# Kernel tuning notes

Hardware: AMD Instinct MI355X
Metric: run time of the kernel (lower is better)

The kernel has to match this reference:

```python
import jax, jax.numpy as jnp
import numpy as np

B, T, E, H = 2, 2048, 1024, 16
Dh = E // H  # head_size = 64


def setup_inputs() -> dict:
    key = jax.random.key(0)
    ks = jax.random.split(key, 6)
    s = E ** -0.5
    x = jax.random.normal(ks[0], (B, T, E), dtype=jnp.float32)
    Wq = jax.random.normal(ks[1], (H, E, Dh), dtype=jnp.float32) * s
    Wk = jax.random.normal(ks[2], (H, E, Dh), dtype=jnp.float32) * s
    Wv = jax.random.normal(ks[3], (H, E, Dh), dtype=jnp.float32) * s
    wo_w = jax.random.normal(ks[4], (E, E), dtype=jnp.float32) * s  # torch Linear weight [out,in]
    wo_b = jax.random.normal(ks[5], (E,), dtype=jnp.float32) * 0.01
    return {"x": x, "Wq": Wq, "Wk": Wk, "Wv": Wv, "wo_w": wo_w, "wo_b": wo_b}


def reference(x, Wq, Wk, Wv, wo_w, wo_b):
    # Batched equivalent of the per-head Python loop: project all heads at once.
    q = jnp.einsum('bte,hed->bhtd', x, Wq)
    k = jnp.einsum('bte,hed->bhtd', x, Wk)
    v = jnp.einsum('bte,hed->bhtd', x, Wv)
    scale = Dh ** -0.5
    scores = jnp.einsum('bhtd,bhsd->bhts', q, k) * scale  # [B,H,T,T]
    causal = jnp.tril(jnp.ones((T, T), dtype=bool))
    scores = jnp.where(causal, scores, jnp.finfo(scores.dtype).min)
    att = jax.nn.softmax(scores, axis=-1)
    out = jnp.einsum('bhts,bhsd->bhtd', att, v)  # [B,H,T,Dh]
    # concat heads (head order along last dim, matching torch.cat over heads)
    out = out.transpose(0, 2, 1, 3).reshape(B, T, E)
    return out @ wo_w.T + wo_b
```

## Files before the change

kernel.cpp:

```cpp
#include <hip/hip_runtime.h>

#define B_ 2
#define T_ 2048
#define E_ 1024
#define H_ 16
#define DH 64

typedef unsigned short u16;
typedef unsigned int u32;
typedef __bf16 bf16x8 __attribute__((ext_vector_type(8)));
typedef float f32x4 __attribute__((ext_vector_type(4)));

__device__ __forceinline__ u16 f2bf(float f) {
  u32 u = __builtin_bit_cast(u32, f);
  u = u + 0x7FFFu + ((u >> 16) & 1u);
  return (u16)(u >> 16);
}
__device__ __forceinline__ float bf2f(u16 v) {
  return __builtin_bit_cast(float, (u32)v << 16);
}
__device__ __forceinline__ bf16x8 ldfrag(const u16* p) { return *(const bf16x8*)p; }

__device__ __forceinline__ void gload_lds16(const u16* g, u16* l) {
  __builtin_amdgcn_global_load_lds((const __attribute__((address_space(1))) u32*)g,
                                   (__attribute__((address_space(3))) u32*)l, 16, 0, 0);
}

__global__ void k_conv_x(const float* __restrict__ src, u16* __restrict__ dst) {
  u32 i = (blockIdx.x * 256u + threadIdx.x) * 8u;
  float4 a = *(const float4*)(src + i);
  float4 b = *(const float4*)(src + i + 4);
  uint4 v;
  v.x = (u32)f2bf(a.x) | ((u32)f2bf(a.y) << 16);
  v.y = (u32)f2bf(a.z) | ((u32)f2bf(a.w) << 16);
  v.z = (u32)f2bf(b.x) | ((u32)f2bf(b.y) << 16);
  v.w = (u32)f2bf(b.z) | ((u32)f2bf(b.w) << 16);
  *(uint4*)(dst + i) = v;
}

__global__ __launch_bounds__(256) void k_conv_wT(const float* __restrict__ Wq, const float* __restrict__ Wk,
                                                 const float* __restrict__ Wv, u16* __restrict__ wT) {
  __shared__ __align__(16) u16 Ls[64][68];
  const int t = threadIdx.x;
  const int e0 = blockIdx.x * 64;
  const int h = blockIdx.y;
  const int which = blockIdx.z;
  const float* src = (which == 0) ? Wq : ((which == 1) ? Wk : Wv);
  const float scale = (which == 0) ? 0.18033688011112042f : 1.0f;
#pragma unroll
  for (int p = 0; p < 4; p++) {
    int idx = p * 256 + t;
    int row = idx >> 4, ch = idx & 15;
    float4 v = *(const float4*)(src + ((size_t)h * E_ + e0 + row) * DH + ch * 4);
    uint2 pk;
    pk.x = (u32)f2bf(v.x * scale) | ((u32)f2bf(v.y * scale) << 16);
    pk.y = (u32)f2bf(v.z * scale) | ((u32)f2bf(v.w * scale) << 16);
    *(uint2*)(&Ls[row][ch * 4]) = pk;
  }
  __syncthreads();
  u16* dst = wT + ((size_t)which * H_ + h) * (DH * E_);
#pragma unroll
  for (int p = 0; p < 4; p++) {
    int idx = p * 256 + t;
    int d = idx >> 4, ec = idx & 15;
    uint2 pk;
    pk.x = (u32)Ls[ec * 4 + 0][d] | ((u32)Ls[ec * 4 + 1][d] << 16);
    pk.y = (u32)Ls[ec * 4 + 2][d] | ((u32)Ls[ec * 4 + 3][d] << 16);
    *(uint2*)(dst + (size_t)d * E_ + e0 + ec * 4) = pk;
  }
}

__global__ __launch_bounds__(256, 3) void k_qkv(const u16* __restrict__ xb, const u16* __restrict__ wT,
                                                u16* __restrict__ Qb, u16* __restrict__ Kb,
                                                u16* __restrict__ VbT) {
  __shared__ __align__(16) u16 As[128 * 64];
  __shared__ __align__(16) u16 Bs[128 * 64];
  const int tid = threadIdx.x;
  const int w = tid >> 6, lane = tid & 63, quad = lane >> 4, lr = lane & 15;
  const int wr = w >> 1, wc = w & 1;
  const int t0 = blockIdx.x * 128;
  const int n0 = blockIdx.y * 128;
  const int sr = lane >> 3, sc = lane & 7;

  f32x4 acc[4][4];
  const f32x4 z4 = {0.f, 0.f, 0.f, 0.f};
#pragma unroll
  for (int i = 0; i < 4; i++)
#pragma unroll
    for (int j = 0; j < 4; j++) acc[i][j] = z4;

  for (int k0 = 0; k0 < E_; k0 += 64) {
    __syncthreads();
#pragma unroll
    for (int ii = 0; ii < 4; ii++) {
      int ra = w * 32 + ii * 8 + sr;
      gload_lds16(xb + (size_t)(t0 + ra) * E_ + k0 + ((sc ^ (ra & 7)) << 3),
                  As + (w * 32 + ii * 8) * 64);
      gload_lds16(wT + (size_t)(n0 + ra) * E_ + k0 + ((sc ^ (ra & 7)) << 3),
                  Bs + (w * 32 + ii * 8) * 64);
    }
    __syncthreads();
#pragma unroll
    for (int kk = 0; kk < 2; kk++) {
      bf16x8 af[4], bfv[4];
#pragma unroll
      for (int rt = 0; rt < 4; rt++) {
        int row = wr * 64 + rt * 16 + lr;
        af[rt] = ldfrag(As + row * 64 + (((kk * 4 + quad) ^ (row & 7)) << 3));
      }
#pragma unroll
      for (int ct = 0; ct < 4; ct++) {
        int row = wc * 64 + ct * 16 + lr;
        bfv[ct] = ldfrag(Bs + row * 64 + (((kk * 4 + quad) ^ (row & 7)) << 3));
      }
#pragma unroll
      for (int rt = 0; rt < 4; rt++)
#pragma unroll
        for (int ct = 0; ct < 4; ct++)
          acc[rt][ct] = __builtin_amdgcn_mfma_f32_16x16x32_bf16(af[rt], bfv[ct], acc[rt][ct], 0, 0, 0);
    }
  }

  const int qkv = n0 >> 10;
  if (qkv < 2) {
    u16* outp = (qkv == 0) ? Qb : Kb;
#pragma unroll
    for (int rt = 0; rt < 4; rt++)
#pragma unroll
      for (int ct = 0; ct < 4; ct++) {
        int n = n0 + wc * 64 + ct * 16 + lr;
        int h = (n >> 6) & 15, d = n & 63;
#pragma unroll
        for (int r = 0; r < 4; r++) {
          int t = t0 + wr * 64 + rt * 16 + quad * 4 + r;
          int bb = t >> 11, tt = t & 2047;
          outp[(((size_t)bb * H_ + h) * T_ + tt) * DH + d] = f2bf(acc[rt][ct][r]);
        }
      }
  } else {
#pragma unroll
    for (int rt = 0; rt < 4; rt++)
#pragma unroll
      for (int ct = 0; ct < 4; ct++) {
        int n = n0 + wc * 64 + ct * 16 + lr;
        int h = (n >> 6) & 15, d = n & 63;
        int t = t0 + wr * 64 + rt * 16 + quad * 4;
        int bb = t >> 11, tt = t & 2047;
        uint2 pk;
        pk.x = (u32)f2bf(acc[rt][ct][0]) | ((u32)f2bf(acc[rt][ct][1]) << 16);
        pk.y = (u32)f2bf(acc[rt][ct][2]) | ((u32)f2bf(acc[rt][ct][3]) << 16);
        *(uint2*)(VbT + (((size_t)bb * H_ + h) * DH + d) * T_ + tt) = pk;
      }
  }
}

__global__ __launch_bounds__(256, 4) void k_attn(const u16* __restrict__ Qb, const u16* __restrict__ Kb,
                                                 const u16* __restrict__ VbT, u16* __restrict__ O0,
                                                 u16* __restrict__ O1, float* __restrict__ Mb,
                                                 float* __restrict__ Lb) {
  __shared__ __align__(16) u16 Qs[64 * 64];
  __shared__ __align__(16) u16 Ks[64 * 64];
  __shared__ __align__(16) u16 Vts[64 * 64];
  __shared__ __align__(16) u16 Ps[64 * 64];
  const int tid = threadIdx.x;
  const int w = tid >> 6, lane = tid & 63, quad = lane >> 4, lr = lane & 15;
  const int l7 = lr & 7;
  const int srow = lane >> 3, schunk = lane & 7;
  const int i = blockIdx.x >> 1, s = blockIdx.x & 1;
  const int h = blockIdx.y, bb = blockIdx.z;
  const u16* qb = Qb + ((size_t)bb * H_ + h) * (size_t)(T_ * DH);
  const u16* kb = Kb + ((size_t)bb * H_ + h) * (size_t)(T_ * DH);
  const u16* vbT = VbT + ((size_t)bb * H_ + h) * (size_t)(T_ * DH);
  const f32x4 z4 = {0.f, 0.f, 0.f, 0.f};

  for (int jb = 0; jb < 2; jb++) {
    const int qt = jb ? i : (31 - i);
    const int sg = jb ? (1 - s) : s;
    const int t0 = qt * 64;
    __syncthreads();
#pragma unroll
    for (int ii = 0; ii < 2; ii++) {
      int r = w * 16 + ii * 8 + srow;
      gload_lds16(qb + (size_t)(t0 + r) * DH + ((schunk ^ (r & 7)) << 3),
                  Qs + (w * 16 + ii * 8) * 64);
    }

    f32x4 o_acc[4];
#pragma unroll
    for (int dt = 0; dt < 4; dt++) o_acc[dt] = z4;
    float m_i = -__builtin_inff(), l_i = 0.f;

    for (int jt = sg; jt <= qt; jt += 2) {
      const int j0 = jt * 64;
      __syncthreads();
#pragma unroll
      for (int ii = 0; ii < 2; ii++) {
        int r = w * 16 + ii * 8 + srow;
        gload_lds16(kb + (size_t)(j0 + r) * DH + ((schunk ^ (r & 7)) << 3),
                    Ks + (w * 16 + ii * 8) * 64);
        gload_lds16(vbT + (size_t)r * T_ + j0 + ((schunk ^ (r & 7)) << 3),
                    Vts + (w * 16 + ii * 8) * 64);
      }
      __syncthreads();

      f32x4 s_acc[4];
#pragma unroll
      for (int st = 0; st < 4; st++) s_acc[st] = z4;
#pragma unroll
      for (int kk = 0; kk < 2; kk++) {
        bf16x8 bq = ldfrag(Qs + (w * 16 + lr) * 64 + (((kk * 4 + quad) ^ l7) << 3));
#pragma unroll
        for (int st = 0; st < 4; st++) {
          bf16x8 ak = ldfrag(Ks + (st * 16 + lr) * 64 + (((kk * 4 + quad) ^ l7) << 3));
          s_acc[st] = __builtin_amdgcn_mfma_f32_16x16x32_bf16(ak, bq, s_acc[st], 0, 0, 0);
        }
      }

      if (jt == qt) {
        int qloc = w * 16 + lr;
#pragma unroll
        for (int st = 0; st < 4; st++) {
          int sbase = st * 16 + quad * 4;
#pragma unroll
          for (int r = 0; r < 4; r++)
            if (sbase + r > qloc) s_acc[st][r] = -__builtin_inff();
        }
      }

      float v01 = fmaxf(fmaxf(s_acc[0][0], s_acc[0][1]), fmaxf(s_acc[0][2], s_acc[0][3]));
      float v23 = fmaxf(fmaxf(s_acc[1][0], s_acc[1][1]), fmaxf(s_acc[1][2], s_acc[1][3]));
      float v45 = fmaxf(fmaxf(s_acc[2][0], s_acc[2][1]), fmaxf(s_acc[2][2], s_acc[2][3]));
      float v67 = fmaxf(fmaxf(s_acc[3][0], s_acc[3][1]), fmaxf(s_acc[3][2], s_acc[3][3]));
      float v = fmaxf(fmaxf(v01, v23), fmaxf(v45, v67));
      v = fmaxf(v, __shfl_xor(v, 16));
      v = fmaxf(v, __shfl_xor(v, 32));
      float mnew = fmaxf(m_i, v);
      float alpha = __builtin_amdgcn_exp2f(m_i - mnew);
      m_i = mnew;
      float rsum = 0.f;
#pragma unroll
      for (int st = 0; st < 4; st++) {
        float p0 = __builtin_amdgcn_exp2f(s_acc[st][0] - m_i);
        float p1 = __builtin_amdgcn_exp2f(s_acc[st][1] - m_i);
        float p2 = __builtin_amdgcn_exp2f(s_acc[st][2] - m_i);
        float p3 = __builtin_amdgcn_exp2f(s_acc[st][3] - m_i);
        rsum += (p0 + p1) + (p2 + p3);
        uint2 pk;
        pk.x = (__builtin_bit_cast(u32, p0) >> 16) | (__builtin_bit_cast(u32, p1) & 0xffff0000u);
        pk.y = (__builtin_bit_cast(u32, p2) >> 16) | (__builtin_bit_cast(u32, p3) & 0xffff0000u);
        *(uint2*)(Ps + (w * 16 + lr) * 64 + (((st * 2 + (quad >> 1)) ^ l7) << 3) + ((quad & 1) << 2)) = pk;
      }
      rsum += __shfl_xor(rsum, 16);
      rsum += __shfl_xor(rsum, 32);
      l_i = l_i * alpha + rsum;
#pragma unroll
      for (int dt = 0; dt < 4; dt++)
#pragma unroll
        for (int r = 0; r < 4; r++) o_acc[dt][r] *= alpha;

#pragma unroll
      for (int kk = 0; kk < 2; kk++) {
        bf16x8 bp = ldfrag(Ps + (w * 16 + lr) * 64 + (((kk * 4 + quad) ^ l7) << 3));
#pragma unroll
        for (int dt = 0; dt < 4; dt++) {
          bf16x8 av = ldfrag(Vts + (dt * 16 + lr) * 64 + (((kk * 4 + quad) ^ l7) << 3));
          o_acc[dt] = __builtin_amdgcn_mfma_f32_16x16x32_bf16(av, bp, o_acc[dt], 0, 0, 0);
        }
      }
    }

    u16* op = (sg == 0) ? O0 : O1;
    float inv = (l_i > 0.f) ? (1.0f / l_i) : 0.f;
    int t = t0 + w * 16 + lr;
    u16* orow = op + ((size_t)bb * T_ + t) * E_ + h * DH;
#pragma unroll
    for (int dt = 0; dt < 4; dt++) {
      uint2 pk;
      pk.x = (u32)f2bf(o_acc[dt][0] * inv) | ((u32)f2bf(o_acc[dt][1] * inv) << 16);
      pk.y = (u32)f2bf(o_acc[dt][2] * inv) | ((u32)f2bf(o_acc[dt][3] * inv) << 16);
      *(uint2*)(orow + dt * 16 + quad * 4) = pk;
    }
    if (quad == 0) {
      int idx = ((sg * B_ + bb) * H_ + h) * T_ + t;
      Mb[idx] = m_i;
      Lb[idx] = l_i;
    }
  }
}

__global__ void k_combine(u16* __restrict__ AO, const u16* __restrict__ O1,
                          const float* __restrict__ Mb, const float* __restrict__ Lb) {
  int idx = blockIdx.x * 256 + threadIdx.x;
  int e0 = idx * 4;
  int bb = e0 >> 21, t = (e0 >> 10) & 2047, hh = (e0 >> 6) & 15;
  int r0 = (bb * H_ + hh) * T_ + t;
  int r1 = r0 + B_ * H_ * T_;
  float m0 = Mb[r0], l0 = Lb[r0], m1 = Mb[r1], l1 = Lb[r1];
  float m = fmaxf(m0, m1);
  float w0 = l0 * __builtin_amdgcn_exp2f(m0 - m);
  float w1 = l1 * __builtin_amdgcn_exp2f(m1 - m);
  float inv = 1.0f / (w0 + w1);
  float a0 = w0 * inv, a1 = w1 * inv;
  uint2 u0 = *(const uint2*)(AO + e0);
  uint2 u1 = *(const uint2*)(O1 + e0);
  float f0 = a0 * bf2f((u16)u0.x) + a1 * bf2f((u16)u1.x);
  float f1 = a0 * bf2f((u16)(u0.x >> 16)) + a1 * bf2f((u16)(u1.x >> 16));
  float f2 = a0 * bf2f((u16)u0.y) + a1 * bf2f((u16)u1.y);
  float f3 = a0 * bf2f((u16)(u0.y >> 16)) + a1 * bf2f((u16)(u1.y >> 16));
  uint2 o;
  o.x = (u32)f2bf(f0) | ((u32)f2bf(f1) << 16);
  o.y = (u32)f2bf(f2) | ((u32)f2bf(f3) << 16);
  *(uint2*)(AO + e0) = o;
}

__global__ __launch_bounds__(256, 3) void k_oproj(const u16* __restrict__ AO, const u16* __restrict__ woB,
                                                  const float* __restrict__ bias, float* __restrict__ out) {
  __shared__ __align__(16) u16 As[128 * 64];
  __shared__ __align__(16) u16 Bs[128 * 64];
  const int tid = threadIdx.x;
  const int w = tid >> 6, lane = tid & 63, quad = lane >> 4, lr = lane & 15;
  const int wr = w >> 1, wc = w & 1;
  const int r0 = blockIdx.x * 128, n0 = blockIdx.y * 128;
  const int sr = lane >> 3, sc = lane & 7;

  f32x4 acc[4][4];
  const f32x4 z4 = {0.f, 0.f, 0.f, 0.f};
#pragma unroll
  for (int i = 0; i < 4; i++)
#pragma unroll
    for (int j = 0; j < 4; j++) acc[i][j] = z4;

  for (int k0 = 0; k0 < E_; k0 += 64) {
    __syncthreads();
#pragma unroll
    for (int ii = 0; ii < 4; ii++) {
      int ra = w * 32 + ii * 8 + sr;
      gload_lds16(AO + (size_t)(r0 + ra) * E_ + k0 + ((sc ^ (ra & 7)) << 3),
                  As + (w * 32 + ii * 8) * 64);
      gload_lds16(woB + (size_t)(n0 + ra) * E_ + k0 + ((sc ^ (ra & 7)) << 3),
                  Bs + (w * 32 + ii * 8) * 64);
    }
    __syncthreads();
#pragma unroll
    for (int kk = 0; kk < 2; kk++) {
      bf16x8 af[4], bfv[4];
#pragma unroll
      for (int rt = 0; rt < 4; rt++) {
        int row = wr * 64 + rt * 16 + lr;
        af[rt] = ldfrag(As + row * 64 + (((kk * 4 + quad) ^ (row & 7)) << 3));
      }
#pragma unroll
      for (int ct = 0; ct < 4; ct++) {
        int row = wc * 64 + ct * 16 + lr;
        bfv[ct] = ldfrag(Bs + row * 64 + (((kk * 4 + quad) ^ (row & 7)) << 3));
      }
#pragma unroll
      for (int rt = 0; rt < 4; rt++)
#pragma unroll
        for (int ct = 0; ct < 4; ct++)
          acc[rt][ct] = __builtin_amdgcn_mfma_f32_16x16x32_bf16(af[rt], bfv[ct], acc[rt][ct], 0, 0, 0);
    }
  }

#pragma unroll
  for (int ct = 0; ct < 4; ct++) {
    float bv = bias[n0 + wc * 64 + ct * 16 + lr];
#pragma unroll
    for (int rt = 0; rt < 4; rt++)
#pragma unroll
      for (int r = 0; r < 4; r++) {
        int row = r0 + wr * 64 + rt * 16 + quad * 4 + r;
        out[(size_t)row * E_ + n0 + wc * 64 + ct * 16 + lr] = acc[rt][ct][r] + bv;
      }
  }
}

extern "C" void kernel_launch(void* const* d_in, const int* in_sizes, int n_in,
                              void* d_out, int out_size, void* d_ws, size_t ws_size,
                              hipStream_t stream) {
  const float* x = (const float*)d_in[0];
  const float* Wq = (const float*)d_in[1];
  const float* Wk = (const float*)d_in[2];
  const float* Wv = (const float*)d_in[3];
  const float* wo_w = (const float*)d_in[4];
  const float* wo_b = (const float*)d_in[5];
  float* out = (float*)d_out;
  char* ws = (char*)d_ws;

  u16* xb  = (u16*)(ws + 0);
  u16* wT  = (u16*)(ws + 8388608);
  u16* woB = (u16*)(ws + 14680064);
  u16* Qb  = (u16*)(ws + 16777216);
  u16* Kb  = (u16*)(ws + 25165824);
  u16* VbT = (u16*)(ws + 33554432);
  u16* AO  = (u16*)(ws + 41943040);
  u16* O1  = xb;
  float* Mb = (float*)(ws + 8388608);
  float* Lb = (float*)(ws + 8912896);

  k_conv_x<<<2048, 256, 0, stream>>>(x, xb);
  k_conv_wT<<<dim3(16, 16, 3), 256, 0, stream>>>(Wq, Wk, Wv, wT);
  k_conv_x<<<512, 256, 0, stream>>>(wo_w, woB);
  k_qkv<<<dim3(32, 24), 256, 0, stream>>>(xb, wT, Qb, Kb, VbT);
  k_attn<<<dim3(32, 16, 2), 256, 0, stream>>>(Qb, Kb, VbT, AO, O1, Mb, Lb);
  k_combine<<<4096, 256, 0, stream>>>(AO, O1, Mb, Lb);
  k_oproj<<<dim3(32, 8), 256, 0, stream>>>(AO, woB, wo_b, out);
}
```

Measured before the change: 181.2 us.

## Fuse conversion kernels, double-buffer K/V in attention, shrink oproj tiles

Merges the three fp32-to-bf16 conversion launches into one kernel that picks its role from the block index, removing two launches. The attention kernel now loads Q fragments straight from global memory into registers. K/V tiles are double-buffered in LDS so the next tile's load overlaps the current tile's compute. The output projection uses 64x128 tiles with 512 blocks instead of 256, giving better CU fill at the cost of less reuse per block. The larger LDS footprint in attention may reduce occupancy.

```diff
diff --git a/kernel.cpp b/kernel.cpp
--- a/kernel.cpp
+++ b/kernel.cpp
@@ -26,31 +26,40 @@
                                    (__attribute__((address_space(3))) u32*)l, 16, 0, 0);
 }
 
-__global__ void k_conv_x(const float* __restrict__ src, u16* __restrict__ dst) {
-  u32 i = (blockIdx.x * 256u + threadIdx.x) * 8u;
-  float4 a = *(const float4*)(src + i);
-  float4 b = *(const float4*)(src + i + 4);
-  uint4 v;
-  v.x = (u32)f2bf(a.x) | ((u32)f2bf(a.y) << 16);
-  v.y = (u32)f2bf(a.z) | ((u32)f2bf(a.w) << 16);
-  v.z = (u32)f2bf(b.x) | ((u32)f2bf(b.y) << 16);
-  v.w = (u32)f2bf(b.z) | ((u32)f2bf(b.w) << 16);
-  *(uint4*)(dst + i) = v;
-}
-
-__global__ __launch_bounds__(256) void k_conv_wT(const float* __restrict__ Wq, const float* __restrict__ Wk,
-                                                 const float* __restrict__ Wv, u16* __restrict__ wT) {
+__global__ __launch_bounds__(256) void k_conv_all(const float* __restrict__ x,
+                                                  const float* __restrict__ Wq,
+                                                  const float* __restrict__ Wk,
+                                                  const float* __restrict__ Wv,
+                                                  const float* __restrict__ wo_w,
+                                                  u16* __restrict__ xb, u16* __restrict__ wT,
+                                                  u16* __restrict__ woB) {
   __shared__ __align__(16) u16 Ls[64][68];
   const int t = threadIdx.x;
-  const int e0 = blockIdx.x * 64;
-  const int h = blockIdx.y;
-  const int which = blockIdx.z;
+  const int bx = blockIdx.x;
+  if (bx < 2048 || bx >= 2816) {
+    const float* src = (bx < 2048) ? x : wo_w;
+    u16* dst = (bx < 2048) ? xb : woB;
+    u32 i = (((bx < 2048) ? bx : (bx - 2816)) * 256u + t) * 8u;
+    float4 a = *(const float4*)(src + i);
+    float4 b = *(const float4*)(src + i + 4);
+    uint4 v;
+    v.x = (u32)f2bf(a.x) | ((u32)f2bf(a.y) << 16);
+    v.y = (u32)f2bf(a.z) | ((u32)f2bf(a.w) << 16);
+    v.z = (u32)f2bf(b.x) | ((u32)f2bf(b.y) << 16);
+    v.w = (u32)f2bf(b.z) | ((u32)f2bf(b.w) << 16);
+    *(uint4*)(dst + i) = v;
+    return;
+  }
+  const int idx = bx - 2048;
+  const int e0 = (idx & 15) * 64;
+  const int h = (idx >> 4) & 15;
+  const int which = idx >> 8;
   const float* src = (which == 0) ? Wq : ((which == 1) ? Wk : Wv);
   const float scale = (which == 0) ? 0.18033688011112042f : 1.0f;
 #pragma unroll
   for (int p = 0; p < 4; p++) {
-    int idx = p * 256 + t;
-    int row = idx >> 4, ch = idx & 15;
+    int id2 = p * 256 + t;
+    int row = id2 >> 4, ch = id2 & 15;
     float4 v = *(const float4*)(src + ((size_t)h * E_ + e0 + row) * DH + ch * 4);
     uint2 pk;
     pk.x = (u32)f2bf(v.x * scale) | ((u32)f2bf(v.y * scale) << 16);
@@ -61,8 +70,8 @@
   u16* dst = wT + ((size_t)which * H_ + h) * (DH * E_);
 #pragma unroll
   for (int p = 0; p < 4; p++) {
-    int idx = p * 256 + t;
-    int d = idx >> 4, ec = idx & 15;
+    int id2 = p * 256 + t;
+    int d = id2 >> 4, ec = id2 & 15;
     uint2 pk;
     pk.x = (u32)Ls[ec * 4 + 0][d] | ((u32)Ls[ec * 4 + 1][d] << 16);
     pk.y = (u32)Ls[ec * 4 + 2][d] | ((u32)Ls[ec * 4 + 3][d] << 16);
@@ -158,10 +167,8 @@
                                                  const u16* __restrict__ VbT, u16* __restrict__ O0,
                                                  u16* __restrict__ O1, float* __restrict__ Mb,
                                                  float* __restrict__ Lb) {
-  __shared__ __align__(16) u16 Qs[64 * 64];
-  __shared__ __align__(16) u16 Ks[64 * 64];
-  __shared__ __align__(16) u16 Vts[64 * 64];
-  __shared__ __align__(16) u16 Ps[64 * 64];
+  __shared__ __align__(16) u16 KV[2][8192];
+  __shared__ __align__(16) u16 Ps[4096];
   const int tid = threadIdx.x;
   const int w = tid >> 6, lane = tid & 63, quad = lane >> 4, lr = lane & 15;
   const int l7 = lr & 7;
@@ -178,42 +185,54 @@
     const int sg = jb ? (1 - s) : s;
     const int t0 = qt * 64;
     __syncthreads();
-#pragma unroll
-    for (int ii = 0; ii < 2; ii++) {
-      int r = w * 16 + ii * 8 + srow;
-      gload_lds16(qb + (size_t)(t0 + r) * DH + ((schunk ^ (r & 7)) << 3),
-                  Qs + (w * 16 + ii * 8) * 64);
-    }
+
+    const u16* qrow = qb + (size_t)(t0 + w * 16 + lr) * DH;
+    bf16x8 bq0 = ldfrag(qrow + quad * 8);
+    bf16x8 bq1 = ldfrag(qrow + 32 + quad * 8);
 
     f32x4 o_acc[4];
 #pragma unroll
     for (int dt = 0; dt < 4; dt++) o_acc[dt] = z4;
     float m_i = -__builtin_inff(), l_i = 0.f;
 
-    for (int jt = sg; jt <= qt; jt += 2) {
-      const int j0 = jt * 64;
-      __syncthreads();
+    int cur = 0;
+    if (sg <= qt) {
+      int j0 = sg * 64;
 #pragma unroll
       for (int ii = 0; ii < 2; ii++) {
         int r = w * 16 + ii * 8 + srow;
         gload_lds16(kb + (size_t)(j0 + r) * DH + ((schunk ^ (r & 7)) << 3),
-                    Ks + (w * 16 + ii * 8) * 64);
+                    KV[0] + (w * 16 + ii * 8) * 64);
         gload_lds16(vbT + (size_t)r * T_ + j0 + ((schunk ^ (r & 7)) << 3),
-                    Vts + (w * 16 + ii * 8) * 64);
-      }
+                    KV[0] + 4096 + (w * 16 + ii * 8) * 64);
+      }
+    }
+
+    for (int jt = sg; jt <= qt; jt += 2) {
       __syncthreads();
+      if (jt + 2 <= qt) {
+        int j0n = (jt + 2) * 64;
+#pragma unroll
+        for (int ii = 0; ii < 2; ii++) {
+          int r = w * 16 + ii * 8 + srow;
+          gload_lds16(kb + (size_t)(j0n + r) * DH + ((schunk ^ (r & 7)) << 3),
+                      KV[cur ^ 1] + (w * 16 + ii * 8) * 64);
+          gload_lds16(vbT + (size_t)r * T_ + j0n + ((schunk ^ (r & 7)) << 3),
+                      KV[cur ^ 1] + 4096 + (w * 16 + ii * 8) * 64);
+        }
+      }
+      const u16* Ks = KV[cur];
+      const u16* Vts = KV[cur] + 4096;
 
       f32x4 s_acc[4];
 #pragma unroll
       for (int st = 0; st < 4; st++) s_acc[st] = z4;
 #pragma unroll
-      for (int kk = 0; kk < 2; kk++) {
-        bf16x8 bq = ldfrag(Qs + (w * 16 + lr) * 64 + (((kk * 4 + quad) ^ l7) << 3));
-#pragma unroll
-        for (int st = 0; st < 4; st++) {
-          bf16x8 ak = ldfrag(Ks + (st * 16 + lr) * 64 + (((kk * 4 + quad) ^ l7) << 3));
-          s_acc[st] = __builtin_amdgcn_mfma_f32_16x16x32_bf16(ak, bq, s_acc[st], 0, 0, 0);
-        }
+      for (int st = 0; st < 4; st++) {
+        bf16x8 ak0 = ldfrag(Ks + (st * 16 + lr) * 64 + ((quad ^ l7) << 3));
+        bf16x8 ak1 = ldfrag(Ks + (st * 16 + lr) * 64 + (((4 + quad) ^ l7) << 3));
+        s_acc[st] = __builtin_amdgcn_mfma_f32_16x16x32_bf16(ak0, bq0, s_acc[st], 0, 0, 0);
+        s_acc[st] = __builtin_amdgcn_mfma_f32_16x16x32_bf16(ak1, bq1, s_acc[st], 0, 0, 0);
       }
 
       if (jt == qt) {
@@ -267,6 +286,7 @@
           o_acc[dt] = __builtin_amdgcn_mfma_f32_16x16x32_bf16(av, bp, o_acc[dt], 0, 0, 0);
         }
       }
+      cur ^= 1;
     }
 
     u16* op = (sg == 0) ? O0 : O1;
@@ -313,64 +333,68 @@
   *(uint2*)(AO + e0) = o;
 }
 
-__global__ __launch_bounds__(256, 3) void k_oproj(const u16* __restrict__ AO, const u16* __restrict__ woB,
+__global__ __launch_bounds__(256, 2) void k_oproj(const u16* __restrict__ AO, const u16* __restrict__ woB,
                                                   const float* __restrict__ bias, float* __restrict__ out) {
-  __shared__ __align__(16) u16 As[128 * 64];
+  __shared__ __align__(16) u16 As[64 * 64];
   __shared__ __align__(16) u16 Bs[128 * 64];
   const int tid = threadIdx.x;
   const int w = tid >> 6, lane = tid & 63, quad = lane >> 4, lr = lane & 15;
-  const int wr = w >> 1, wc = w & 1;
-  const int r0 = blockIdx.x * 128, n0 = blockIdx.y * 128;
+  const int r0 = blockIdx.x * 64, n0 = blockIdx.y * 128;
   const int sr = lane >> 3, sc = lane & 7;
 
-  f32x4 acc[4][4];
+  f32x4 acc[4][2];
   const f32x4 z4 = {0.f, 0.f, 0.f, 0.f};
 #pragma unroll
   for (int i = 0; i < 4; i++)
 #pragma unroll
-    for (int j = 0; j < 4; j++) acc[i][j] = z4;
+    for (int j = 0; j < 2; j++) acc[i][j] = z4;
 
   for (int k0 = 0; k0 < E_; k0 += 64) {
     __syncthreads();
 #pragma unroll
+    for (int ii = 0; ii < 2; ii++) {
+      int ra = w * 16 + ii * 8 + sr;
+      gload_lds16(AO + (size_t)(r0 + ra) * E_ + k0 + ((sc ^ (ra & 7)) << 3),
+                  As + (w * 16 + ii * 8) * 64);
+    }
+#pragma unroll
     for (int ii = 0; ii < 4; ii++) {
-      int ra = w * 32 + ii * 8 + sr;
-      gload_lds16(AO + (size_t)(r0 + ra) * E_ + k0 + ((sc ^ (ra & 7)) << 3),
-                  As + (w * 32 + ii * 8) * 64);
-      gload_lds16(woB + (size_t)(n0 + ra) * E_ + k0 + ((sc ^ (ra & 7)) << 3),
+      int rb = w * 32 + ii * 8 + sr;
+      gload_lds16(woB + (size_t)(n0 + rb) * E_ + k0 + ((sc ^ (rb & 7)) << 3),
                   Bs + (w * 32 + ii * 8) * 64);
     }
     __syncthreads();
 #pragma unroll
     for (int kk = 0; kk < 2; kk++) {
-      bf16x8 af[4], bfv[4];
+      bf16x8 af[4], bfv[2];
 #pragma unroll
       for (int rt = 0; rt < 4; rt++) {
-        int row = wr * 64 + rt * 16 + lr;
+        int row = rt * 16 + lr;
         af[rt] = ldfrag(As + row * 64 + (((kk * 4 + quad) ^ (row & 7)) << 3));
       }
 #pragma unroll
-      for (int ct = 0; ct < 4; ct++) {
-        int row = wc * 64 + ct * 16 + lr;
+      for (int ct = 0; ct < 2; ct++) {
+        int row = w * 32 + ct * 16 + lr;
         bfv[ct] = ldfrag(Bs + row * 64 + (((kk * 4 + quad) ^ (row & 7)) << 3));
       }
 #pragma unroll
       for (int rt = 0; rt < 4; rt++)
 #pragma unroll
-        for (int ct = 0; ct < 4; ct++)
+        for (int ct = 0; ct < 2; ct++)
           acc[rt][ct] = __builtin_amdgcn_mfma_f32_16x16x32_bf16(af[rt], bfv[ct], acc[rt][ct], 0, 0, 0);
     }
   }
 
 #pragma unroll
-  for (int ct = 0; ct < 4; ct++) {
-    float bv = bias[n0 + wc * 64 + ct * 16 + lr];
+  for (int ct = 0; ct < 2; ct++) {
+    int col = n0 + w * 32 + ct * 16 + lr;
+    float bv = bias[col];
 #pragma unroll
     for (int rt = 0; rt < 4; rt++)
 #pragma unroll
       for (int r = 0; r < 4; r++) {
-        int row = r0 + wr * 64 + rt * 16 + quad * 4 + r;
-        out[(size_t)row * E_ + n0 + wc * 64 + ct * 16 + lr] = acc[rt][ct][r] + bv;
+        int row = r0 + rt * 16 + quad * 4 + r;
+        out[(size_t)row * E_ + col] = acc[rt][ct][r] + bv;
       }
   }
 }
@@ -398,11 +422,9 @@
   float* Mb = (float*)(ws + 8388608);
   float* Lb = (float*)(ws + 8912896);
 
-  k_conv_x<<<2048, 256, 0, stream>>>(x, xb);
-  k_conv_wT<<<dim3(16, 16, 3), 256, 0, stream>>>(Wq, Wk, Wv, wT);
-  k_conv_x<<<512, 256, 0, stream>>>(wo_w, woB);
+  k_conv_all<<<3328, 256, 0, stream>>>(x, Wq, Wk, Wv, wo_w, xb, wT, woB);
   k_qkv<<<dim3(32, 24), 256, 0, stream>>>(xb, wT, Qb, Kb, VbT);
   k_attn<<<dim3(32, 16, 2), 256, 0, stream>>>(Qb, Kb, VbT, AO, O1, Mb, Lb);
   k_combine<<<4096, 256, 0, stream>>>(AO, O1, Mb, Lb);
-  k_oproj<<<dim3(32, 8), 256, 0, stream>>>(AO, woB, wo_b, out);
-}
+  k_oproj<<<dim3(64, 8), 256, 0, stream>>>(AO, woB, wo_b, out);
+}
```

New measurement: 180.7 us. Within noise of the previous version (-0.3%).
